# Kernel optimization log

Hardware: AMD Instinct MI355X
Metric: run time of the kernel (lower is better)

Reference implementation:

```python
import jax, jax.numpy as jnp
import numpy as np

N_NODES = 100000
N_EDGES = 1600000
N_GRAPHS = 64
VOCAB = 50000
D = 128
EPS = 1e-5


def setup_inputs() -> dict:
    key = jax.random.key(0)
    ks = jax.random.split(key, 24)
    tokens = jax.random.randint(ks[0], (N_NODES,), 0, VOCAB)
    src = jax.random.randint(ks[1], (N_EDGES,), 0, N_NODES)
    dst = jax.random.randint(ks[2], (N_EDGES,), 0, N_NODES)
    graph_ids = jnp.sort(jax.random.randint(ks[3], (N_NODES,), 0, N_GRAPHS))
    s = 1.0 / np.sqrt(D)
    inp = {
        'tokens': tokens, 'src': src, 'dst': dst, 'graph_ids': graph_ids,
        'embed': jax.random.normal(ks[4], (VOCAB, D), jnp.float32),
        'W1': jax.random.normal(ks[5], (D, D), jnp.float32) * s,
        'b1': jnp.zeros((D,), jnp.float32),
        'g1': jnp.ones((D,), jnp.float32), 'be1': jnp.zeros((D,), jnp.float32),
        'W2': jax.random.normal(ks[6], (D, D), jnp.float32) * s,
        'b2': jnp.zeros((D,), jnp.float32),
        'g2': jnp.ones((D,), jnp.float32), 'be2': jnp.zeros((D,), jnp.float32),
        'W3': jax.random.normal(ks[7], (D, D), jnp.float32) * s,
        'b3': jnp.zeros((D,), jnp.float32),
        'g3': jnp.ones((D,), jnp.float32), 'be3': jnp.zeros((D,), jnp.float32),
        'fcW1': jax.random.normal(ks[8], (D, D // 2), jnp.float32) * s,
        'fcb1': jnp.zeros((D // 2,), jnp.float32),
        'fcW2': jax.random.normal(ks[9], (D // 2, 2), jnp.float32) * (1.0 / np.sqrt(D // 2)),
        'fcb2': jnp.zeros((2,), jnp.float32),
    }
    return inp


def _graph_conv(h, src, dst, norm_src, norm_dst, W, b):
    # DGL GraphConv, norm='both': D_out^{-1/2} -> sum-aggregate -> D_in^{-1/2} -> linear
    msg = (h * norm_src[:, None])[src]                      # [E, D]
    agg = jax.ops.segment_sum(msg, dst, num_segments=N_NODES)
    return (agg * norm_dst[:, None]) @ W + b


def _bn_relu(h, gamma, beta):
    mu = jnp.mean(h, axis=0)
    var = jnp.mean((h - mu) ** 2, axis=0)                   # biased var (torch BN)
    return jax.nn.relu((h - mu) * jax.lax.rsqrt(var + EPS) * gamma + beta)


def reference(tokens, src, dst, graph_ids, embed,
              W1, b1, g1, be1, W2, b2, g2, be2, W3, b3, g3, be3,
              fcW1, fcb1, fcW2, fcb2):
    ones_e = jnp.ones((N_EDGES,), jnp.float32)
    deg_out = jnp.maximum(jax.ops.segment_sum(ones_e, src, num_segments=N_NODES), 1.0)
    deg_in = jnp.maximum(jax.ops.segment_sum(ones_e, dst, num_segments=N_NODES), 1.0)
    norm_src = jax.lax.rsqrt(deg_out)
    norm_dst = jax.lax.rsqrt(deg_in)

    h = embed[tokens]                                        # [N, D]
    h = _bn_relu(_graph_conv(h, src, dst, norm_src, norm_dst, W1, b1), g1, be1)
    h = _bn_relu(_graph_conv(h, src, dst, norm_src, norm_dst, W2, b2), g2, be2)
    h = _bn_relu(_graph_conv(h, src, dst, norm_src, norm_dst, W3, b3), g3, be3)

    # dgl.mean_nodes per graph
    sums = jax.ops.segment_sum(h, graph_ids, num_segments=N_GRAPHS)  # [G, D]
    cnts = jnp.maximum(jax.ops.segment_sum(jnp.ones((N_NODES,), jnp.float32), graph_ids, num_segments=N_GRAPHS), 1.0)
    hg = sums / cnts[:, None]

    hg = jax.nn.relu(hg @ fcW1 + fcb1)                       # dropout = identity (eval)
    return hg @ fcW2 + fcb2                                  # [G, 2]
```

## Files before the change

kernel.cpp:

```cpp
#include <hip/hip_runtime.h>

#define N_NODES 100000
#define N_EDGES 1600000
#define N_GRAPHS 64
#define DIM 128
#define BN_EPS 1e-5f
#define EPAD 2000000

#define NB_SENT 977
#define NB_WPREP 192
#define NB_HIST 391
#define NB_ZERO 40
#define NBUCK 782
#define NG (NBUCK * NB_HIST)
#define NB_SCANG2 2389
#define BUCK_RESERVE 388

#define AT_STRIDE 136

typedef unsigned short ushort_t;
typedef unsigned char uchar_t;
typedef unsigned int uint_t;
typedef __attribute__((ext_vector_type(8))) short bf16x8;
typedef __attribute__((ext_vector_type(4))) float f32x4;

__device__ __forceinline__ float bfl(uint_t u) {
    union { uint_t i; float f; } v; v.i = u << 16; return v.f;
}
__device__ __forceinline__ float bfh(uint_t u) {
    union { uint_t i; float f; } v; v.i = u & 0xffff0000u; return v.f;
}
__device__ __forceinline__ ushort_t f2bf(float f) {
    union { float f; uint_t i; } v; v.f = f;
    uint_t x = v.i;
    return (ushort_t)((x + 0x7fffu + ((x >> 16) & 1u)) >> 16);
}
__device__ __forceinline__ uint_t pack2(float lo, float hi) {
    return ((uint_t)f2bf(hi) << 16) | (uint_t)f2bf(lo);
}

__global__ void k_front(const int* __restrict__ src, const int* __restrict__ dst,
                        ushort_t* __restrict__ bufA, int* __restrict__ esrc,
                        const float* __restrict__ w1, const float* __restrict__ w2,
                        const float* __restrict__ w3, ushort_t* __restrict__ wbt,
                        int* __restrict__ GG, int* __restrict__ zp, int zwords) {
    __shared__ int hh[NBUCK];
    __shared__ int hh2[NBUCK];
    int b = blockIdx.x;
    int t = threadIdx.x;
    if (b < NB_SENT) {
        int i0 = (b * 256 + t) * 8;
        int4 sv = make_int4(N_NODES, N_NODES, N_NODES, N_NODES);
        if (i0 + 8 <= EPAD) {
            *(int4*)(esrc + i0) = sv;
            *(int4*)(esrc + i0 + 4) = sv;
        } else {
            for (int i = i0; i < EPAD; ++i) esrc[i] = N_NODES;
        }
        if (b == 0 && t < 64)
            ((uint_t*)(bufA + (size_t)N_NODES * DIM))[t] = 0u;
        return;
    }
    b -= NB_SENT;
    if (b < NB_WPREP) {
        int i = b * 256 + t;
        int l = i >> 14;
        int idx = i & (DIM * DIM - 1);
        int n = idx >> 7, k = idx & (DIM - 1);
        const float* wsrc = (l == 0) ? w1 : (l == 1) ? w2 : w3;
        wbt[i] = f2bf(wsrc[k * DIM + n]);
        return;
    }
    b -= NB_WPREP;
    if (b < NB_HIST) {
        for (int k = t; k < NBUCK; k += 256) { hh[k] = 0; hh2[k] = 0; }
        __syncthreads();
        int e0 = b * 4096;
        int e1 = min(e0 + 4096, N_EDGES);
        for (int i = e0 + t; i < e1; i += 256) {
            atomicAdd(&hh[dst[i] >> 7], 1);
            atomicAdd(&hh2[src[i] >> 7], 1);
        }
        __syncthreads();
        for (int k = t; k < NBUCK; k += 256) {
            GG[k * NB_HIST + b] = hh[k];
            GG[NG + k * NB_HIST + b] = hh2[k];
        }
        return;
    }
    b -= NB_HIST;
    {
        int i = b * 256 + t;
        if (i < zwords) zp[i] = 0;
    }
}

__global__ void k_scanA(const int* __restrict__ GG, int* __restrict__ Gs,
                        int* __restrict__ partials) {
    __shared__ int s[256];
    int t = threadIdx.x;
    int i = blockIdx.x * 256 + t;
    int v = (i < 2 * NG) ? GG[i] : 0;
    s[t] = v;
    __syncthreads();
    for (int off = 1; off < 256; off <<= 1) {
        int add = (t >= off) ? s[t - off] : 0;
        __syncthreads();
        s[t] += add;
        __syncthreads();
    }
    if (i < 2 * NG) Gs[i + 1] = s[t];
    if (t == 255) partials[blockIdx.x] = s[t];
}

__global__ void k_scanB(const int* __restrict__ partials, int* __restrict__ Gs) {
    __shared__ int s[256];
    int t = threadIdx.x;
    int p = 0;
    for (int j = t; j < (int)blockIdx.x; j += 256) p += partials[j];
    s[t] = p;
    __syncthreads();
    for (int off = 128; off > 0; off >>= 1) {
        if (t < off) s[t] += s[t + off];
        __syncthreads();
    }
    int prefix = s[0];
    int i = blockIdx.x * 256 + t;
    if (i < 2 * NG) Gs[i + 1] += prefix;
    if (blockIdx.x == 0 && t == 0) Gs[0] = 0;
}

__global__ void k_pass2(const int* __restrict__ src, const int* __restrict__ dst,
                        const int* __restrict__ Gs, uint_t* __restrict__ Cpk,
                        uchar_t* __restrict__ Cls) {
    __shared__ int cur[NBUCK];
    __shared__ int cur2[NBUCK];
    int b = blockIdx.x;
    int t = threadIdx.x;
    for (int k = t; k < NBUCK; k += 256) {
        cur[k] = Gs[k * NB_HIST + b];
        cur2[k] = Gs[NG + k * NB_HIST + b] - N_EDGES;
    }
    __syncthreads();
    int e0 = b * 4096;
    int e1 = min(e0 + 4096, N_EDGES);
    for (int i = e0 + t; i < e1; i += 256) {
        int d = dst[i];
        int s = src[i];
        int slot = atomicAdd(&cur[d >> 7], 1);
        Cpk[slot] = (uint_t)s | ((uint_t)(d & 127) << 17);
        int slot2 = atomicAdd(&cur2[s >> 7], 1);
        Cls[slot2] = (uchar_t)(s & 127);
    }
}

__global__ void k_fine(const uint_t* __restrict__ Cpk, const uchar_t* __restrict__ Cls,
                       const int* __restrict__ Gs,
                       const int* __restrict__ tokens, const float* __restrict__ embed,
                       int* __restrict__ esrc, int* __restrict__ rowptr,
                       int* __restrict__ pdeg, float* __restrict__ ns,
                       float* __restrict__ nd, ushort_t* __restrict__ bufA) {
    __shared__ int hcnt[128];
    __shared__ int hstart[128];
    __shared__ float lns[128];
    int b = blockIdx.x;
    int t = threadIdx.x;
    if (b < NBUCK) {
        int k = b;
        int node0 = k * 128;
        int nn = min(128, N_NODES - node0);
        int S = Gs[k * NB_HIST];
        int E = Gs[(k + 1) * NB_HIST];
        if (t < 128) hcnt[t] = 0;
        __syncthreads();
        for (int i = S + t; i < E; i += 256) atomicAdd(&hcnt[Cpk[i] >> 17], 1);
        __syncthreads();
        if (t == 0) {
            int acc = 0;
            for (int n = 0; n < nn; ++n) {
                hstart[n] = acc;
                acc += (hcnt[n] + 3) & ~3;
            }
        }
        __syncthreads();
        int base = (k * BUCK_RESERVE + S + 3) & ~3;
        if (t < nn) {
            int node = node0 + t;
            rowptr[node] = base + hstart[t];
            pdeg[node] = (hcnt[t] + 3) & ~3;
            nd[node] = rsqrtf(fmaxf((float)hcnt[t], 1.0f));
        }
        __syncthreads();
        for (int i = S + t; i < E; i += 256) {
            uint_t pk = Cpk[i];
            int slot = atomicAdd(&hstart[pk >> 17], 1);
            esrc[base + slot] = (int)(pk & 0x1FFFFu);
        }
    } else {
        int k = b - NBUCK;
        int node0 = k * 128;
        int nn = min(128, N_NODES - node0);
        int S = Gs[NG + k * NB_HIST] - N_EDGES;
        int E = Gs[NG + (k + 1) * NB_HIST] - N_EDGES;
        if (t < 128) hcnt[t] = 0;
        __syncthreads();
        for (int i = S + t; i < E; i += 256) atomicAdd(&hcnt[Cls[i]], 1);
        __syncthreads();
        if (t < nn) {
            float v = rsqrtf(fmaxf((float)hcnt[t], 1.0f));
            ns[node0 + t] = v;
            lns[t] = v;
        }
        if (k == 0 && t == 0) ns[N_NODES] = 0.f;
        __syncthreads();
        for (int slot = t; slot < nn * 16; slot += 256) {
            int nloc = slot >> 4, sub = slot & 15;
            int node = node0 + nloc;
            float s = lns[nloc];
            const float* ep = embed + (size_t)tokens[node] * DIM + sub * 8;
            float4 a = *(const float4*)ep;
            float4 c = *(const float4*)(ep + 4);
            uint4 o;
            o.x = pack2(a.x * s, a.y * s);
            o.y = pack2(a.z * s, a.w * s);
            o.z = pack2(c.x * s, c.y * s);
            o.w = pack2(c.z * s, c.w * s);
            *(uint4*)(bufA + (size_t)node * DIM + sub * 8) = o;
        }
    }
}

__global__ void k_prescale(const ushort_t* __restrict__ yin, const float* __restrict__ ns,
                           const float* __restrict__ bnsum, const float* __restrict__ bnsq,
                           const float* __restrict__ g, const float* __restrict__ be,
                           ushort_t* __restrict__ xout) {
    __shared__ float sa[DIM], sc[DIM];
    int t = threadIdx.x;
    if (t < DIM) {
        float mu = bnsum[t] * (1.0f / N_NODES);
        float var = bnsq[t] * (1.0f / N_NODES) - mu * mu;
        float rstd = rsqrtf(var + BN_EPS);
        float a = g[t] * rstd;
        sa[t] = a;
        sc[t] = be[t] - mu * a;
    }
    __syncthreads();
    int gid = blockIdx.x * 256 + t;
    int node = gid >> 4, sub = gid & 15;
    float s = ns[node];
    uint4 u = *(const uint4*)(yin + (size_t)node * DIM + sub * 8);
    float v[8] = {bfl(u.x), bfh(u.x), bfl(u.y), bfh(u.y),
                  bfl(u.z), bfh(u.z), bfl(u.w), bfh(u.w)};
    const float* a = sa + sub * 8;
    const float* c = sc + sub * 8;
#pragma unroll
    for (int i = 0; i < 8; ++i) v[i] = fmaxf(fmaf(v[i], a[i], c[i]), 0.f) * s;
    uint4 o;
    o.x = pack2(v[0], v[1]); o.y = pack2(v[2], v[3]);
    o.z = pack2(v[4], v[5]); o.w = pack2(v[6], v[7]);
    *(uint4*)(xout + (size_t)node * DIM + sub * 8) = o;
}

__global__ __launch_bounds__(256) void k_agggemm(const ushort_t* __restrict__ hs,
        const int* __restrict__ rowptr, const int* __restrict__ pdeg,
        const int* __restrict__ esrc, const float* __restrict__ nd,
        const ushort_t* __restrict__ wbt, const float* __restrict__ bias,
        ushort_t* __restrict__ y,
        float* __restrict__ bnsum, float* __restrict__ bnsq) {
    __shared__ ushort_t at[64 * AT_STRIDE];
    __shared__ float csum[DIM], csq[DIM];
    int tid = threadIdx.x;
    int wave = tid >> 6;
    int lane = tid & 63;
    if (tid < DIM) { csum[tid] = 0.f; csq[tid] = 0.f; }
    __syncthreads();

    int bnode = blockIdx.x * 64 + wave * 16;
    int quad = lane >> 4;
    int m16 = lane & 15;

    const ushort_t* hrow = hs + (size_t)m16 * 8;

    int rpv = 0, epv = 0;
    float ndv = 0.f;
    if (lane < 16) {
        int nnode = bnode + lane;
        if (nnode < N_NODES) {
            rpv = rowptr[nnode];
            epv = rpv + pdeg[nnode];
            ndv = nd[nnode];
        }
    }
    int ws = __shfl(rpv, 0);
    int T = (__shfl(epv, 15) - ws) >> 2;

#define FEATLD(ix) (*(const uint4*)(hrow + (size_t)(ix) * DIM))
#define ACCU(F)                                                     \
    {                                                               \
        a[0] += bfl((F).x); a[1] += bfh((F).x);                     \
        a[2] += bfl((F).y); a[3] += bfh((F).y);                     \
        a[4] += bfl((F).z); a[5] += bfh((F).z);                     \
        a[6] += bfl((F).w); a[7] += bfh((F).w);                     \
    }
#define FLUSH()                                                     \
    {                                                               \
        float nv = __shfl(ndv, ni);                                 \
        _Pragma("unroll")                                           \
        for (int j = 0; j < 8; ++j) {                               \
            a[j] += __shfl_xor(a[j], 16);                           \
            a[j] += __shfl_xor(a[j], 32);                           \
        }                                                           \
        if (quad == 0) {                                            \
            uint4 o;                                                \
            o.x = pack2(a[0] * nv, a[1] * nv);                      \
            o.y = pack2(a[2] * nv, a[3] * nv);                      \
            o.z = pack2(a[4] * nv, a[5] * nv);                      \
            o.w = pack2(a[6] * nv, a[7] * nv);                      \
            *(uint4*)&at[(wave * 16 + ni) * AT_STRIDE + m16 * 8] = o; \
        }                                                           \
        _Pragma("unroll")                                           \
        for (int j = 0; j < 8; ++j) a[j] = 0.f;                     \
    }
#define BCHK()                                                      \
    while (ni < 16 && pos >= end_cur) {                             \
        FLUSH();                                                    \
        ++ni;                                                       \
        end_cur = __shfl(epv, ni < 16 ? ni : 15);                   \
    }

    float a[8] = {0.f, 0.f, 0.f, 0.f, 0.f, 0.f, 0.f, 0.f};
    int ni = 0;
    int end_cur = __shfl(epv, 0);
    int pos = ws + 4;

    int sl = ws + quad;
    int i0 = esrc[sl], i1 = esrc[sl + 4], i2 = esrc[sl + 8], i3 = esrc[sl + 12];
    uint4 f0 = FEATLD(i0), f1 = FEATLD(i1), f2 = FEATLD(i2), f3 = FEATLD(i3);
    i0 = esrc[sl + 16]; i1 = esrc[sl + 20]; i2 = esrc[sl + 24]; i3 = esrc[sl + 28];
    sl += 32;

    int t = 0;
    for (; t + 4 <= T; t += 4) {
        { int n_ = esrc[sl]; sl += 4; ACCU(f0); f0 = FEATLD(i0); i0 = n_; BCHK(); pos += 4; }
        { int n_ = esrc[sl]; sl += 4; ACCU(f1); f1 = FEATLD(i1); i1 = n_; BCHK(); pos += 4; }
        { int n_ = esrc[sl]; sl += 4; ACCU(f2); f2 = FEATLD(i2); i2 = n_; BCHK(); pos += 4; }
        { int n_ = esrc[sl]; sl += 4; ACCU(f3); f3 = FEATLD(i3); i3 = n_; BCHK(); pos += 4; }
    }
    if (t + 0 < T) { ACCU(f0); BCHK(); pos += 4; }
    if (t + 1 < T) { ACCU(f1); BCHK(); pos += 4; }
    if (t + 2 < T) { ACCU(f2); BCHK(); pos += 4; }
    while (ni < 16) { FLUSH(); ++ni; }
#undef BCHK
#undef FLUSH
#undef ACCU
#undef FEATLD

    f32x4 acc[8];
#pragma unroll
    for (int nb = 0; nb < 8; ++nb) acc[nb] = (f32x4)(0.f);

    const ushort_t* ap = &at[(wave * 16 + m16) * AT_STRIDE + quad * 8];
#pragma unroll
    for (int k0b = 0; k0b < 4; ++k0b) {
        bf16x8 af = *(const bf16x8*)(ap + k0b * 32);
#pragma unroll
        for (int nb = 0; nb < 8; ++nb) {
            int ncol = nb * 16 + m16;
            bf16x8 bfg = *(const bf16x8*)(wbt + (size_t)ncol * DIM + k0b * 32 + quad * 8);
            acc[nb] = __builtin_amdgcn_mfma_f32_16x16x32_bf16(af, bfg, acc[nb], 0, 0, 0);
        }
    }

#pragma unroll
    for (int nb = 0; nb < 8; ++nb) {
        int col = nb * 16 + m16;
        float bcol = bias[col];
        float ps = 0.f, pq = 0.f;
#pragma unroll
        for (int reg = 0; reg < 4; ++reg) {
            int r = bnode + quad * 4 + reg;
            if (r < N_NODES) {
                float v = acc[nb][reg] + bcol;
                ps += v; pq += v * v;
                y[(size_t)r * DIM + col] = f2bf(v);
            }
        }
        atomicAdd(&csum[col], ps);
        atomicAdd(&csq[col], pq);
    }
    __syncthreads();
    if (tid < DIM) {
        atomicAdd(&bnsum[tid], csum[tid]);
        atomicAdd(&bnsq[tid], csq[tid]);
    }
}

#define POOL_NODES 128
__global__ void k_pool(const ushort_t* __restrict__ yin, const int* __restrict__ gids,
                       const float* __restrict__ bnsum, const float* __restrict__ bnsq,
                       const float* __restrict__ g, const float* __restrict__ be,
                       float* __restrict__ pool, int* __restrict__ cnt) {
    __shared__ int h[N_GRAPHS];
    int col = threadIdx.x;
    float mu = bnsum[col] * (1.0f / N_NODES);
    float var = bnsq[col] * (1.0f / N_NODES) - mu * mu;
    float rstd = rsqrtf(var + BN_EPS);
    float a = g[col] * rstd;
    float c = be[col] - mu * a;
    if (col < N_GRAPHS) h[col] = 0;
    __syncthreads();
    int base = blockIdx.x * POOL_NODES;
    int end = min(base + POOL_NODES, N_NODES);
    for (int n = base + col; n < end; n += 128) atomicAdd(&h[gids[n]], 1);
    __syncthreads();
    if (col < N_GRAPHS && h[col]) atomicAdd(&cnt[col], h[col]);
    float acc = 0.f;
    int cur = gids[base];
    for (int n = base; n < end; ++n) {
        int gg = gids[n];
        if (gg != cur) {
            atomicAdd(&pool[(size_t)cur * DIM + col], acc);
            acc = 0.f;
            cur = gg;
        }
        uint_t u = *(const uint_t*)(yin + (size_t)n * DIM + (col & ~1));
        float v = (col & 1) ? bfh(u) : bfl(u);
        acc += fmaxf(fmaf(v, a, c), 0.f);
    }
    atomicAdd(&pool[(size_t)cur * DIM + col], acc);
}

__global__ void k_final(const float* __restrict__ pool, const int* __restrict__ cnt,
                        const float* __restrict__ fcW1, const float* __restrict__ fcb1,
                        const float* __restrict__ fcW2, const float* __restrict__ fcb2,
                        float* __restrict__ out) {
    __shared__ float hg[DIM];
    __shared__ float z[64];
    int g = blockIdx.x;
    int t = threadIdx.x;
    float cf = fmaxf((float)cnt[g], 1.0f);
    hg[t] = pool[(size_t)g * DIM + t] / cf;
    __syncthreads();
    if (t < 64) {
        float acc = fcb1[t];
        for (int k = 0; k < DIM; ++k)
            acc += hg[k] * fcW1[k * 64 + t];
        z[t] = fmaxf(acc, 0.f);
    }
    __syncthreads();
    if (t < 2) {
        float acc = fcb2[t];
        for (int k = 0; k < 64; ++k)
            acc += z[k] * fcW2[k * 2 + t];
        out[g * 2 + t] = acc;
    }
}

extern "C" void kernel_launch(void* const* d_in, const int* in_sizes, int n_in,
                              void* d_out, int out_size, void* d_ws, size_t ws_size,
                              hipStream_t stream) {
    const int* tokens = (const int*)d_in[0];
    const int* src = (const int*)d_in[1];
    const int* dst = (const int*)d_in[2];
    const int* gids = (const int*)d_in[3];
    const float* embed = (const float*)d_in[4];
    const float* W1 = (const float*)d_in[5];
    const float* b1 = (const float*)d_in[6];
    const float* g1 = (const float*)d_in[7];
    const float* be1 = (const float*)d_in[8];
    const float* W2 = (const float*)d_in[9];
    const float* b2 = (const float*)d_in[10];
    const float* g2 = (const float*)d_in[11];
    const float* be2 = (const float*)d_in[12];
    const float* W3 = (const float*)d_in[13];
    const float* b3 = (const float*)d_in[14];
    const float* g3 = (const float*)d_in[15];
    const float* be3 = (const float*)d_in[16];
    const float* fcW1 = (const float*)d_in[17];
    const float* fcb1 = (const float*)d_in[18];
    const float* fcW2 = (const float*)d_in[19];
    const float* fcb2 = (const float*)d_in[20];
    float* out = (float*)d_out;

    char* w = (char*)d_ws;
    auto alloc = [&](size_t bytes) {
        void* p = (void*)w;
        w += (bytes + 255) & ~(size_t)255;
        return p;
    };
    ushort_t* bufH = (ushort_t*)alloc((size_t)(N_NODES + 1) * DIM * 2);
    ushort_t* bufA = (ushort_t*)alloc((size_t)(N_NODES + 1) * DIM * 2);
    ushort_t* bufY = (ushort_t*)alloc((size_t)(N_NODES + 1) * DIM * 2);
    int* esrc = (int*)alloc((size_t)EPAD * 4);
    int* rowptr = (int*)alloc((size_t)N_NODES * 4);
    int* pdeg = (int*)alloc((size_t)N_NODES * 4);
    float* ns = (float*)alloc((size_t)(N_NODES + 1) * 4);
    float* nd = (float*)alloc((size_t)N_NODES * 4);
    ushort_t* wbt = (ushort_t*)alloc(3 * DIM * DIM * 2);
    int* GG = (int*)alloc((size_t)(2 * NG) * 4);
    int* Gs = (int*)alloc((size_t)(2 * NG + 1) * 4);
    int* partials = (int*)alloc(4096 * 4);
    uint_t* Cpk = (uint_t*)alloc((size_t)N_EDGES * 4);
    uchar_t* Cls = (uchar_t*)alloc((size_t)N_EDGES);
    char* zstart = w;
    float* bnsum = (float*)alloc(3 * DIM * 4);
    float* bnsq = (float*)alloc(3 * DIM * 4);
    float* pool = (float*)alloc((size_t)N_GRAPHS * DIM * 4);
    int* cnt = (int*)alloc((size_t)N_GRAPHS * 4);
    int zwords = (int)((size_t)(w - zstart) / 4);

    k_front<<<NB_SENT + NB_WPREP + NB_HIST + NB_ZERO, 256, 0, stream>>>(
        src, dst, bufA, esrc, W1, W2, W3, wbt, GG, (int*)zstart, zwords);
    k_scanA<<<NB_SCANG2, 256, 0, stream>>>(GG, Gs, partials);
    k_scanB<<<NB_SCANG2, 256, 0, stream>>>(partials, Gs);
    k_pass2<<<NB_HIST, 256, 0, stream>>>(src, dst, Gs, Cpk, Cls);
    k_fine<<<2 * NBUCK, 256, 0, stream>>>(Cpk, Cls, Gs, tokens, embed,
                                          esrc, rowptr, pdeg, ns, nd, bufA);

    int nb_fused = (N_NODES + 63) / 64;
    int nb_ps = 6250;

    k_agggemm<<<nb_fused, 256, 0, stream>>>(bufA, rowptr, pdeg, esrc, nd,
                                            wbt, b1, bufY, bnsum, bnsq);
    k_prescale<<<nb_ps, 256, 0, stream>>>(bufY, ns, bnsum, bnsq, g1, be1, bufA);
    k_agggemm<<<nb_fused, 256, 0, stream>>>(bufA, rowptr, pdeg, esrc, nd,
                                            wbt + (size_t)DIM * DIM, b2, bufH,
                                            bnsum + DIM, bnsq + DIM);
    k_prescale<<<nb_ps, 256, 0, stream>>>(bufH, ns, bnsum + DIM, bnsq + DIM, g2, be2, bufA);
    k_agggemm<<<nb_fused, 256, 0, stream>>>(bufA, rowptr, pdeg, esrc, nd,
                                            wbt + (size_t)2 * DIM * DIM, b3, bufY,
                                            bnsum + 2 * DIM, bnsq + 2 * DIM);

    k_pool<<<(N_NODES + POOL_NODES - 1) / POOL_NODES, DIM, 0, stream>>>(
        bufY, gids, bnsum + 2 * DIM, bnsq + 2 * DIM, g3, be3, pool, cnt);
    k_final<<<N_GRAPHS, DIM, 0, stream>>>(pool, cnt, fcW1, fcb1, fcW2, fcb2, out);
}
```

Baseline: 604.0 us.

## Compute out-degree with global atomics instead of a second bucket sort

The out-degree (source) histogram no longer goes through a two-level bucket counting sort with a scan, a scatter pass and a fine histogram. Each edge now does a global atomicAdd on deg[src], and k_fine reads it directly to compute norm_src and fold the embedding gather into the same blocks. This halves the scan size, drops the Cls scatter, and halves the k_fine grid. In exchange it adds 1.6M global atomics to random addresses and a memset before the first kernel.

```diff
diff --git a/kernel.cpp b/kernel.cpp
--- a/kernel.cpp
+++ b/kernel.cpp
@@ -13,7 +13,7 @@
 #define NB_ZERO 40
 #define NBUCK 782
 #define NG (NBUCK * NB_HIST)
-#define NB_SCANG2 2389
+#define NB_SCANG 1195
 #define BUCK_RESERVE 388
 
 #define AT_STRIDE 136
@@ -43,9 +43,9 @@
                         ushort_t* __restrict__ bufA, int* __restrict__ esrc,
                         const float* __restrict__ w1, const float* __restrict__ w2,
                         const float* __restrict__ w3, ushort_t* __restrict__ wbt,
-                        int* __restrict__ GG, int* __restrict__ zp, int zwords) {
+                        int* __restrict__ GG, int* __restrict__ deg,
+                        int* __restrict__ zp, int zwords) {
     __shared__ int hh[NBUCK];
-    __shared__ int hh2[NBUCK];
     int b = blockIdx.x;
     int t = threadIdx.x;
     if (b < NB_SENT) {
@@ -73,19 +73,17 @@
     }
     b -= NB_WPREP;
     if (b < NB_HIST) {
-        for (int k = t; k < NBUCK; k += 256) { hh[k] = 0; hh2[k] = 0; }
+        for (int k = t; k < NBUCK; k += 256) hh[k] = 0;
         __syncthreads();
         int e0 = b * 4096;
         int e1 = min(e0 + 4096, N_EDGES);
         for (int i = e0 + t; i < e1; i += 256) {
             atomicAdd(&hh[dst[i] >> 7], 1);
-            atomicAdd(&hh2[src[i] >> 7], 1);
+            atomicAdd(&deg[src[i]], 1);
         }
         __syncthreads();
-        for (int k = t; k < NBUCK; k += 256) {
+        for (int k = t; k < NBUCK; k += 256)
             GG[k * NB_HIST + b] = hh[k];
-            GG[NG + k * NB_HIST + b] = hh2[k];
-        }
         return;
     }
     b -= NB_HIST;
@@ -100,7 +98,7 @@
     __shared__ int s[256];
     int t = threadIdx.x;
     int i = blockIdx.x * 256 + t;
-    int v = (i < 2 * NG) ? GG[i] : 0;
+    int v = (i < NG) ? GG[i] : 0;
     s[t] = v;
     __syncthreads();
     for (int off = 1; off < 256; off <<= 1) {
@@ -109,7 +107,7 @@
         s[t] += add;
         __syncthreads();
     }
-    if (i < 2 * NG) Gs[i + 1] = s[t];
+    if (i < NG) Gs[i + 1] = s[t];
     if (t == 255) partials[blockIdx.x] = s[t];
 }
 
@@ -126,21 +124,17 @@
     }
     int prefix = s[0];
     int i = blockIdx.x * 256 + t;
-    if (i < 2 * NG) Gs[i + 1] += prefix;
+    if (i < NG) Gs[i + 1] += prefix;
     if (blockIdx.x == 0 && t == 0) Gs[0] = 0;
 }
 
 __global__ void k_pass2(const int* __restrict__ src, const int* __restrict__ dst,
-                        const int* __restrict__ Gs, uint_t* __restrict__ Cpk,
-                        uchar_t* __restrict__ Cls) {
+                        const int* __restrict__ Gs, uint_t* __restrict__ Cpk) {
     __shared__ int cur[NBUCK];
-    __shared__ int cur2[NBUCK];
     int b = blockIdx.x;
     int t = threadIdx.x;
-    for (int k = t; k < NBUCK; k += 256) {
+    for (int k = t; k < NBUCK; k += 256)
         cur[k] = Gs[k * NB_HIST + b];
-        cur2[k] = Gs[NG + k * NB_HIST + b] - N_EDGES;
-    }
     __syncthreads();
     int e0 = b * 4096;
     int e1 = min(e0 + 4096, N_EDGES);
@@ -149,13 +143,11 @@
         int s = src[i];
         int slot = atomicAdd(&cur[d >> 7], 1);
         Cpk[slot] = (uint_t)s | ((uint_t)(d & 127) << 17);
-        int slot2 = atomicAdd(&cur2[s >> 7], 1);
-        Cls[slot2] = (uchar_t)(s & 127);
-    }
-}
-
-__global__ void k_fine(const uint_t* __restrict__ Cpk, const uchar_t* __restrict__ Cls,
-                       const int* __restrict__ Gs,
+    }
+}
+
+__global__ void k_fine(const uint_t* __restrict__ Cpk, const int* __restrict__ Gs,
+                       const int* __restrict__ deg,
                        const int* __restrict__ tokens, const float* __restrict__ embed,
                        int* __restrict__ esrc, int* __restrict__ rowptr,
                        int* __restrict__ pdeg, float* __restrict__ ns,
@@ -163,70 +155,54 @@
     __shared__ int hcnt[128];
     __shared__ int hstart[128];
     __shared__ float lns[128];
-    int b = blockIdx.x;
-    int t = threadIdx.x;
-    if (b < NBUCK) {
-        int k = b;
-        int node0 = k * 128;
-        int nn = min(128, N_NODES - node0);
-        int S = Gs[k * NB_HIST];
-        int E = Gs[(k + 1) * NB_HIST];
-        if (t < 128) hcnt[t] = 0;
-        __syncthreads();
-        for (int i = S + t; i < E; i += 256) atomicAdd(&hcnt[Cpk[i] >> 17], 1);
-        __syncthreads();
-        if (t == 0) {
-            int acc = 0;
-            for (int n = 0; n < nn; ++n) {
-                hstart[n] = acc;
-                acc += (hcnt[n] + 3) & ~3;
-            }
-        }
-        __syncthreads();
-        int base = (k * BUCK_RESERVE + S + 3) & ~3;
-        if (t < nn) {
-            int node = node0 + t;
-            rowptr[node] = base + hstart[t];
-            pdeg[node] = (hcnt[t] + 3) & ~3;
-            nd[node] = rsqrtf(fmaxf((float)hcnt[t], 1.0f));
-        }
-        __syncthreads();
-        for (int i = S + t; i < E; i += 256) {
-            uint_t pk = Cpk[i];
-            int slot = atomicAdd(&hstart[pk >> 17], 1);
-            esrc[base + slot] = (int)(pk & 0x1FFFFu);
-        }
-    } else {
-        int k = b - NBUCK;
-        int node0 = k * 128;
-        int nn = min(128, N_NODES - node0);
-        int S = Gs[NG + k * NB_HIST] - N_EDGES;
-        int E = Gs[NG + (k + 1) * NB_HIST] - N_EDGES;
-        if (t < 128) hcnt[t] = 0;
-        __syncthreads();
-        for (int i = S + t; i < E; i += 256) atomicAdd(&hcnt[Cls[i]], 1);
-        __syncthreads();
-        if (t < nn) {
-            float v = rsqrtf(fmaxf((float)hcnt[t], 1.0f));
-            ns[node0 + t] = v;
-            lns[t] = v;
-        }
-        if (k == 0 && t == 0) ns[N_NODES] = 0.f;
-        __syncthreads();
-        for (int slot = t; slot < nn * 16; slot += 256) {
-            int nloc = slot >> 4, sub = slot & 15;
-            int node = node0 + nloc;
-            float s = lns[nloc];
-            const float* ep = embed + (size_t)tokens[node] * DIM + sub * 8;
-            float4 a = *(const float4*)ep;
-            float4 c = *(const float4*)(ep + 4);
-            uint4 o;
-            o.x = pack2(a.x * s, a.y * s);
-            o.y = pack2(a.z * s, a.w * s);
-            o.z = pack2(c.x * s, c.y * s);
-            o.w = pack2(c.z * s, c.w * s);
-            *(uint4*)(bufA + (size_t)node * DIM + sub * 8) = o;
-        }
+    int k = blockIdx.x;
+    int t = threadIdx.x;
+    int node0 = k * 128;
+    int nn = min(128, N_NODES - node0);
+    int S = Gs[k * NB_HIST];
+    int E = Gs[(k + 1) * NB_HIST];
+    if (t < 128) hcnt[t] = 0;
+    __syncthreads();
+    for (int i = S + t; i < E; i += 256) atomicAdd(&hcnt[Cpk[i] >> 17], 1);
+    __syncthreads();
+    if (t == 0) {
+        int acc = 0;
+        for (int n = 0; n < nn; ++n) {
+            hstart[n] = acc;
+            acc += (hcnt[n] + 3) & ~3;
+        }
+    }
+    __syncthreads();
+    int base = (k * BUCK_RESERVE + S + 3) & ~3;
+    if (t < nn) {
+        int node = node0 + t;
+        rowptr[node] = base + hstart[t];
+        pdeg[node] = (hcnt[t] + 3) & ~3;
+        nd[node] = rsqrtf(fmaxf((float)hcnt[t], 1.0f));
+        float v = rsqrtf(fmaxf((float)deg[node], 1.0f));
+        ns[node] = v;
+        lns[t] = v;
+    }
+    if (k == 0 && t == 0) ns[N_NODES] = 0.f;
+    __syncthreads();
+    for (int i = S + t; i < E; i += 256) {
+        uint_t pk = Cpk[i];
+        int slot = atomicAdd(&hstart[pk >> 17], 1);
+        esrc[base + slot] = (int)(pk & 0x1FFFFu);
+    }
+    for (int slot = t; slot < nn * 16; slot += 256) {
+        int nloc = slot >> 4, sub = slot & 15;
+        int node = node0 + nloc;
+        float s = lns[nloc];
+        const float* ep = embed + (size_t)tokens[node] * DIM + sub * 8;
+        float4 a = *(const float4*)ep;
+        float4 c = *(const float4*)(ep + 4);
+        uint4 o;
+        o.x = pack2(a.x * s, a.y * s);
+        o.y = pack2(a.z * s, a.w * s);
+        o.z = pack2(c.x * s, c.y * s);
+        o.w = pack2(c.z * s, c.w * s);
+        *(uint4*)(bufA + (size_t)node * DIM + sub * 8) = o;
     }
 }
 
@@ -496,12 +472,12 @@
     int* pdeg = (int*)alloc((size_t)N_NODES * 4);
     float* ns = (float*)alloc((size_t)(N_NODES + 1) * 4);
     float* nd = (float*)alloc((size_t)N_NODES * 4);
+    int* deg = (int*)alloc((size_t)N_NODES * 4);
     ushort_t* wbt = (ushort_t*)alloc(3 * DIM * DIM * 2);
-    int* GG = (int*)alloc((size_t)(2 * NG) * 4);
-    int* Gs = (int*)alloc((size_t)(2 * NG + 1) * 4);
+    int* GG = (int*)alloc((size_t)NG * 4);
+    int* Gs = (int*)alloc((size_t)(NG + 1) * 4);
     int* partials = (int*)alloc(4096 * 4);
     uint_t* Cpk = (uint_t*)alloc((size_t)N_EDGES * 4);
-    uchar_t* Cls = (uchar_t*)alloc((size_t)N_EDGES);
     char* zstart = w;
     float* bnsum = (float*)alloc(3 * DIM * 4);
     float* bnsq = (float*)alloc(3 * DIM * 4);
@@ -509,13 +485,14 @@
     int* cnt = (int*)alloc((size_t)N_GRAPHS * 4);
     int zwords = (int)((size_t)(w - zstart) / 4);
 
+    hipMemsetAsync(deg, 0, (size_t)N_NODES * 4, stream);
     k_front<<<NB_SENT + NB_WPREP + NB_HIST + NB_ZERO, 256, 0, stream>>>(
-        src, dst, bufA, esrc, W1, W2, W3, wbt, GG, (int*)zstart, zwords);
-    k_scanA<<<NB_SCANG2, 256, 0, stream>>>(GG, Gs, partials);
-    k_scanB<<<NB_SCANG2, 256, 0, stream>>>(partials, Gs);
-    k_pass2<<<NB_HIST, 256, 0, stream>>>(src, dst, Gs, Cpk, Cls);
-    k_fine<<<2 * NBUCK, 256, 0, stream>>>(Cpk, Cls, Gs, tokens, embed,
-                                          esrc, rowptr, pdeg, ns, nd, bufA);
+        src, dst, bufA, esrc, W1, W2, W3, wbt, GG, deg, (int*)zstart, zwords);
+    k_scanA<<<NB_SCANG, 256, 0, stream>>>(GG, Gs, partials);
+    k_scanB<<<NB_SCANG, 256, 0, stream>>>(partials, Gs);
+    k_pass2<<<NB_HIST, 256, 0, stream>>>(src, dst, Gs, Cpk);
+    k_fine<<<NBUCK, 256, 0, stream>>>(Cpk, Gs, deg, tokens, embed,
+                                      esrc, rowptr, pdeg, ns, nd, bufA);
 
     int nb_fused = (N_NODES + 63) / 64;
     int nb_ps = 6250;
```

Result: slower. 636.2 us (+5.3%).
